# Kernel optimization log

Measured on AMD Instinct MI355X. Metric: run time of the kernel, lower is better.

## Reference

```python
import jax, jax.numpy as jnp
import numpy as np

NUM_MODULES = 4
EXPERTS_PER_MODULE = 4
TOTAL_EXPERTS = NUM_MODULES * EXPERTS_PER_MODULE
TOP_K = 4
NORM_TOPK_PROB = True
T = 32768
D = 1536


def setup_inputs() -> dict:
    key = jax.random.key(0)
    k1, k2, k3 = jax.random.split(key, 3)
    hidden_states = jax.random.normal(k1, (T, D), dtype=jnp.float32)
    # nn.Linear weights: (out_features, in_features)
    Wm = jax.random.normal(k2, (NUM_MODULES, D), dtype=jnp.float32) * 0.02
    We = jax.random.normal(k3, (TOTAL_EXPERTS, D), dtype=jnp.float32) * 0.02
    return {"hidden_states": hidden_states, "Wm": Wm, "We": We}


def reference(hidden_states, Wm, We):
    Tn = hidden_states.shape[0]
    # Stage 1: module routing
    module_logits = jnp.einsum('td,md->tm', hidden_states, Wm)  # (T, num_modules)
    module_probs = jax.nn.softmax(module_logits.astype(jnp.float32), axis=-1)
    # Stage 2: expert routing, grouped per module (intra-module softmax)
    expert_logits = jnp.einsum('td,ed->te', hidden_states, We)  # (T, total_experts)
    expert_logits = expert_logits.reshape(Tn, NUM_MODULES, EXPERTS_PER_MODULE)
    expert_probs = jax.nn.softmax(expert_logits.astype(jnp.float32), axis=-1)
    # Combined hierarchical distribution
    combined_probs = (module_probs[:, :, None] * expert_probs).reshape(Tn, TOTAL_EXPERTS)
    # Top-k over flat combined distribution
    top_k_weights, top_k_indices = jax.lax.top_k(combined_probs, TOP_K)
    if NORM_TOPK_PROB:
        top_k_weights = top_k_weights / (jnp.sum(top_k_weights, axis=-1, keepdims=True) + 1e-8)
    top_k_weights = top_k_weights.astype(hidden_states.dtype)
    return combined_probs, top_k_weights, top_k_indices
```

## Files before the change

### kernel.cpp

```cpp
#include <hip/hip_runtime.h>
#include <math.h>


#define DD 1536
#define NM 4
#define NE 16
#define NW 20
#define RPB 128
#define NWAVE 8
#define NTHR (NWAVE * 64)
#define CPW 192
#define CHUNK 16
#define HS_FLOATS (RPB * CHUNK)

typedef float v4f __attribute__((ext_vector_type(4)));

union SharedMem {
    float stage[NWAVE * HS_FLOATS];
    float xch[NW * NTHR * 2];
};

__global__ __launch_bounds__(NTHR)
void router_kernel(const float* __restrict__ hs,
                   const float* __restrict__ Wm,
                   const float* __restrict__ We,
                   float* __restrict__ out,
                   int T)
{
    __shared__ SharedMem sm;
    const int tid  = threadIdx.x;
    const int wv   = tid >> 6;
    const int lane = tid & 63;
    const int rowBlock = blockIdx.x * RPB;
    const int colStart = __builtin_amdgcn_readfirstlane(wv * CPW);

    float acc0[NW], acc1[NW];
#pragma unroll
    for (int e = 0; e < NW; e++) { acc0[e] = 0.f; acc1[e] = 0.f; }

    const int srow = lane >> 2;
    const int p    = lane & 3;
    const int sw   = (lane >> 3) & 3;
    const int gcol = ((p ^ sw) << 2);
    const float* dmaBase = hs + (size_t)(rowBlock + srow) * DD + colStart + gcol;

    const int myHsOff = __builtin_amdgcn_readfirstlane(wv * HS_FLOATS);
    const float* WeBase = We + colStart;
    const float* WmBase = Wm + colStart;
    const int rsw = ((lane >> 1) & 3);

    for (int c = 0; c < CPW; c += CHUNK) {
        asm volatile("s_waitcnt lgkmcnt(0)" ::: "memory");
#pragma unroll
        for (int i = 0; i < 8; i++) {
            const float* src = dmaBase + (size_t)(i * 16) * DD + c;
            __builtin_amdgcn_global_load_lds(
                (const __attribute__((address_space(1))) void*)src,
                (__attribute__((address_space(3))) void*)&sm.stage[myHsOff + i * 256],
                16, 0, 0);
        }
        asm volatile("s_waitcnt vmcnt(0)" ::: "memory");

#pragma unroll
        for (int g = 0; g < 4; g++) {
            const int sg = ((g ^ rsw) << 2);
            v4f h0 = *(const v4f*)&sm.stage[myHsOff + (lane << 4) + sg];
            v4f h1 = *(const v4f*)&sm.stage[myHsOff + 1024 + (lane << 4) + sg];
#pragma unroll
            for (int e = 0; e < NE; e++) {
                v4f w = *(const v4f*)(WeBase + e * DD + c + (g << 2));
                acc0[e] += h0.x * w.x + h0.y * w.y + h0.z * w.z + h0.w * w.w;
                acc1[e] += h1.x * w.x + h1.y * w.y + h1.z * w.z + h1.w * w.w;
            }
#pragma unroll
            for (int m = 0; m < NM; m++) {
                v4f w = *(const v4f*)(WmBase + m * DD + c + (g << 2));
                acc0[16 + m] += h0.x * w.x + h0.y * w.y + h0.z * w.z + h0.w * w.w;
                acc1[16 + m] += h1.x * w.x + h1.y * w.y + h1.z * w.z + h1.w * w.w;
            }
        }
    }

    __syncthreads();
#pragma unroll
    for (int e = 0; e < NW; e++) {
        sm.xch[e * (NTHR * 2) + tid]        = acc0[e];
        sm.xch[e * (NTHR * 2) + NTHR + tid] = acc1[e];
    }
    __syncthreads();

    if (wv < 2) {
        const int half = wv * NTHR;
        float logit[NW];
#pragma unroll
        for (int e = 0; e < NW; e++) {
            float s = 0.f;
#pragma unroll
            for (int w = 0; w < NWAVE; w++)
                s += sm.xch[e * (NTHR * 2) + half + w * 64 + lane];
            logit[e] = s;
        }

        float mmax = logit[16];
#pragma unroll
        for (int m = 1; m < NM; m++) mmax = fmaxf(mmax, logit[16 + m]);
        float mexp[NM], msum = 0.f;
#pragma unroll
        for (int m = 0; m < NM; m++) { mexp[m] = expf(logit[16 + m] - mmax); msum += mexp[m]; }

        float comb[NE];
#pragma unroll
        for (int m = 0; m < NM; m++) {
            float mprob = mexp[m] / msum;
            float emax = logit[m * 4];
#pragma unroll
            for (int j = 1; j < 4; j++) emax = fmaxf(emax, logit[m * 4 + j]);
            float ee[4], esum = 0.f;
#pragma unroll
            for (int j = 0; j < 4; j++) { ee[j] = expf(logit[m * 4 + j] - emax); esum += ee[j]; }
            float scale = mprob / esum;
#pragma unroll
            for (int j = 0; j < 4; j++) comb[m * 4 + j] = ee[j] * scale;
        }

        const int row = rowBlock + wv * 64 + lane;
        float4* cw = (float4*)(out + (size_t)row * 16);
        cw[0] = make_float4(comb[0],  comb[1],  comb[2],  comb[3]);
        cw[1] = make_float4(comb[4],  comb[5],  comb[6],  comb[7]);
        cw[2] = make_float4(comb[8],  comb[9],  comb[10], comb[11]);
        cw[3] = make_float4(comb[12], comb[13], comb[14], comb[15]);

        float tv[4]; int ti[4];
        unsigned mask = 0;
#pragma unroll
        for (int k = 0; k < 4; k++) {
            float best = -1.f; int bi = 0;
#pragma unroll
            for (int i = 0; i < NE; i++) {
                bool avail = !((mask >> i) & 1u);
                if (avail && comb[i] > best) { best = comb[i]; bi = i; }
            }
            tv[k] = best; ti[k] = bi; mask |= 1u << bi;
        }
        float s = tv[0] + tv[1] + tv[2] + tv[3] + 1e-8f;

        const size_t wOff = (size_t)T * 16;
        const size_t iOff = (size_t)T * 20;
        float4* ww = (float4*)(out + wOff + (size_t)row * 4);
        *ww = make_float4(tv[0] / s, tv[1] / s, tv[2] / s, tv[3] / s);
        float4* iw = (float4*)(out + iOff + (size_t)row * 4);
        *iw = make_float4((float)ti[0], (float)ti[1], (float)ti[2], (float)ti[3]);
    }
}

extern "C" void kernel_launch(void* const* d_in, const int* in_sizes, int n_in,
                              void* d_out, int out_size, void* d_ws, size_t ws_size,
                              hipStream_t stream)
{
    const float* hs = (const float*)d_in[0];
    const float* Wm = (const float*)d_in[1];
    const float* We = (const float*)d_in[2];
    float* out = (float*)d_out;
    const int T = in_sizes[0] / DD;
    router_kernel<<<T / RPB, NTHR, 0, stream>>>(hs, Wm, We, out, T);
}
```

Baseline: 362.3 us.

## Stage router weights in LDS and stream hidden states directly with shuffle reductions

Each block first copies all 20x1536 router weights (We and Wm) into LDS. Each wave then streams hidden-state rows straight from global memory with register prefetch, with 16 lanes splitting the columns of one row. Partial sums are combined with xor shuffles instead of a shared-memory cross-wave exchange. This removes the global_load_lds staging, the per-chunk waits and the large reduction buffer, but every block now reloads 120KB of weights and occupancy is limited by that LDS footprint.

```diff
diff --git a/kernel.cpp b/kernel.cpp
--- a/kernel.cpp
+++ b/kernel.cpp
@@ -7,18 +7,11 @@
 #define NE 16
 #define NW 20
 #define RPB 128
-#define NWAVE 8
-#define NTHR (NWAVE * 64)
-#define CPW 192
-#define CHUNK 16
-#define HS_FLOATS (RPB * CHUNK)
+#define NTHR 512
+#define NJ 24
+#define WLDS_F (NJ * NW * 64)
 
 typedef float v4f __attribute__((ext_vector_type(4)));
-
-union SharedMem {
-    float stage[NWAVE * HS_FLOATS];
-    float xch[NW * NTHR * 2];
-};
 
 __global__ __launch_bounds__(NTHR)
 void router_kernel(const float* __restrict__ hs,
@@ -27,129 +20,152 @@
                    float* __restrict__ out,
                    int T)
 {
-    __shared__ SharedMem sm;
+    __shared__ __align__(16) float wl[WLDS_F];
     const int tid  = threadIdx.x;
     const int wv   = tid >> 6;
     const int lane = tid & 63;
+    const int q    = lane & 15;
+    const int g    = lane >> 4;
     const int rowBlock = blockIdx.x * RPB;
-    const int colStart = __builtin_amdgcn_readfirstlane(wv * CPW);
-
-    float acc0[NW], acc1[NW];
-#pragma unroll
-    for (int e = 0; e < NW; e++) { acc0[e] = 0.f; acc1[e] = 0.f; }
-
-    const int srow = lane >> 2;
-    const int p    = lane & 3;
-    const int sw   = (lane >> 3) & 3;
-    const int gcol = ((p ^ sw) << 2);
-    const float* dmaBase = hs + (size_t)(rowBlock + srow) * DD + colStart + gcol;
-
-    const int myHsOff = __builtin_amdgcn_readfirstlane(wv * HS_FLOATS);
-    const float* WeBase = We + colStart;
-    const float* WmBase = Wm + colStart;
-    const int rsw = ((lane >> 1) & 3);
-
-    for (int c = 0; c < CPW; c += CHUNK) {
-        asm volatile("s_waitcnt lgkmcnt(0)" ::: "memory");
-#pragma unroll
-        for (int i = 0; i < 8; i++) {
-            const float* src = dmaBase + (size_t)(i * 16) * DD + c;
-            __builtin_amdgcn_global_load_lds(
-                (const __attribute__((address_space(1))) void*)src,
-                (__attribute__((address_space(3))) void*)&sm.stage[myHsOff + i * 256],
-                16, 0, 0);
-        }
-        asm volatile("s_waitcnt vmcnt(0)" ::: "memory");
 
 #pragma unroll
-        for (int g = 0; g < 4; g++) {
-            const int sg = ((g ^ rsw) << 2);
-            v4f h0 = *(const v4f*)&sm.stage[myHsOff + (lane << 4) + sg];
-            v4f h1 = *(const v4f*)&sm.stage[myHsOff + 1024 + (lane << 4) + sg];
-#pragma unroll
-            for (int e = 0; e < NE; e++) {
-                v4f w = *(const v4f*)(WeBase + e * DD + c + (g << 2));
-                acc0[e] += h0.x * w.x + h0.y * w.y + h0.z * w.z + h0.w * w.w;
-                acc1[e] += h1.x * w.x + h1.y * w.y + h1.z * w.z + h1.w * w.w;
-            }
-#pragma unroll
-            for (int m = 0; m < NM; m++) {
-                v4f w = *(const v4f*)(WmBase + m * DD + c + (g << 2));
-                acc0[16 + m] += h0.x * w.x + h0.y * w.y + h0.z * w.z + h0.w * w.w;
-                acc1[16 + m] += h1.x * w.x + h1.y * w.y + h1.z * w.z + h1.w * w.w;
-            }
-        }
-    }
-
-    __syncthreads();
-#pragma unroll
-    for (int e = 0; e < NW; e++) {
-        sm.xch[e * (NTHR * 2) + tid]        = acc0[e];
-        sm.xch[e * (NTHR * 2) + NTHR + tid] = acc1[e];
+    for (int i = 0; i < 15; i++) {
+        const int off  = tid * 4 + i * 2048;
+        const int j    = off / 1280;
+        const int rem  = off - j * 1280;
+        const int e    = rem >> 6;
+        const int qcol = rem & 63;
+        const int col  = j * 64 + qcol;
+        v4f w = (e < NE) ? *(const v4f*)(We + (size_t)e * DD + col)
+                         : *(const v4f*)(Wm + (size_t)(e - NE) * DD + col);
+        *(v4f*)&wl[off] = w;
     }
     __syncthreads();
 
-    if (wv < 2) {
-        const int half = wv * NTHR;
-        float logit[NW];
+#pragma unroll 1
+    for (int p = 0; p < 2; p++) {
+        const int rA = rowBlock + p * 64 + wv * 8 + g;
+        const float* hsA = hs + (size_t)rA * DD + q * 4;
+        const float* hsB = hsA + 4 * DD;
+
+        float accA[NW], accB[NW];
+#pragma unroll
+        for (int e = 0; e < NW; e++) { accA[e] = 0.f; accB[e] = 0.f; }
+
+        v4f a0 = *(const v4f*)(hsA);
+        v4f b0 = *(const v4f*)(hsB);
+        v4f a1 = *(const v4f*)(hsA + 64);
+        v4f b1 = *(const v4f*)(hsB + 64);
+
+#pragma unroll 1
+        for (int j = 0; j < NJ; j += 2) {
+            v4f a2, b2, a3, b3;
+            if (j + 2 < NJ) {
+                a2 = *(const v4f*)(hsA + (size_t)(j + 2) * 64);
+                b2 = *(const v4f*)(hsB + (size_t)(j + 2) * 64);
+                a3 = *(const v4f*)(hsA + (size_t)(j + 3) * 64);
+                b3 = *(const v4f*)(hsB + (size_t)(j + 3) * 64);
+            }
+            {
+                const float* wb = &wl[j * 1280 + q * 4];
+#pragma unroll
+                for (int e = 0; e < NW; e++) {
+                    v4f w = *(const v4f*)(wb + e * 64);
+                    accA[e] = fmaf(a0.x, w.x, accA[e]);
+                    accA[e] = fmaf(a0.y, w.y, accA[e]);
+                    accA[e] = fmaf(a0.z, w.z, accA[e]);
+                    accA[e] = fmaf(a0.w, w.w, accA[e]);
+                    accB[e] = fmaf(b0.x, w.x, accB[e]);
+                    accB[e] = fmaf(b0.y, w.y, accB[e]);
+                    accB[e] = fmaf(b0.z, w.z, accB[e]);
+                    accB[e] = fmaf(b0.w, w.w, accB[e]);
+                }
+            }
+            {
+                const float* wb = &wl[(j + 1) * 1280 + q * 4];
+#pragma unroll
+                for (int e = 0; e < NW; e++) {
+                    v4f w = *(const v4f*)(wb + e * 64);
+                    accA[e] = fmaf(a1.x, w.x, accA[e]);
+                    accA[e] = fmaf(a1.y, w.y, accA[e]);
+                    accA[e] = fmaf(a1.z, w.z, accA[e]);
+                    accA[e] = fmaf(a1.w, w.w, accA[e]);
+                    accB[e] = fmaf(b1.x, w.x, accB[e]);
+                    accB[e] = fmaf(b1.y, w.y, accB[e]);
+                    accB[e] = fmaf(b1.z, w.z, accB[e]);
+                    accB[e] = fmaf(b1.w, w.w, accB[e]);
+                }
+            }
+            a0 = a2; b0 = b2; a1 = a3; b1 = b3;
+        }
+
 #pragma unroll
         for (int e = 0; e < NW; e++) {
-            float s = 0.f;
-#pragma unroll
-            for (int w = 0; w < NWAVE; w++)
-                s += sm.xch[e * (NTHR * 2) + half + w * 64 + lane];
-            logit[e] = s;
+            accA[e] += __shfl_xor(accA[e], 1);
+            accA[e] += __shfl_xor(accA[e], 2);
+            accA[e] += __shfl_xor(accA[e], 4);
+            accA[e] += __shfl_xor(accA[e], 8);
+            accB[e] += __shfl_xor(accB[e], 1);
+            accB[e] += __shfl_xor(accB[e], 2);
+            accB[e] += __shfl_xor(accB[e], 4);
+            accB[e] += __shfl_xor(accB[e], 8);
         }
 
-        float mmax = logit[16];
+        if (q < 2) {
+            float logit[NW];
 #pragma unroll
-        for (int m = 1; m < NM; m++) mmax = fmaxf(mmax, logit[16 + m]);
-        float mexp[NM], msum = 0.f;
+            for (int e = 0; e < NW; e++) logit[e] = q ? accB[e] : accA[e];
+            const int row = rA + (q ? 4 : 0);
+
+            float mmax = logit[16];
 #pragma unroll
-        for (int m = 0; m < NM; m++) { mexp[m] = expf(logit[16 + m] - mmax); msum += mexp[m]; }
+            for (int m = 1; m < NM; m++) mmax = fmaxf(mmax, logit[16 + m]);
+            float mexp[NM], msum = 0.f;
+#pragma unroll
+            for (int m = 0; m < NM; m++) { mexp[m] = expf(logit[16 + m] - mmax); msum += mexp[m]; }
 
-        float comb[NE];
+            float comb[NE];
 #pragma unroll
-        for (int m = 0; m < NM; m++) {
-            float mprob = mexp[m] / msum;
-            float emax = logit[m * 4];
+            for (int m = 0; m < NM; m++) {
+                float mprob = mexp[m] / msum;
+                float emax = logit[m * 4];
 #pragma unroll
-            for (int j = 1; j < 4; j++) emax = fmaxf(emax, logit[m * 4 + j]);
-            float ee[4], esum = 0.f;
+                for (int jj = 1; jj < 4; jj++) emax = fmaxf(emax, logit[m * 4 + jj]);
+                float ee[4], esum = 0.f;
 #pragma unroll
-            for (int j = 0; j < 4; j++) { ee[j] = expf(logit[m * 4 + j] - emax); esum += ee[j]; }
-            float scale = mprob / esum;
+                for (int jj = 0; jj < 4; jj++) { ee[jj] = expf(logit[m * 4 + jj] - emax); esum += ee[jj]; }
+                float scale = mprob / esum;
 #pragma unroll
-            for (int j = 0; j < 4; j++) comb[m * 4 + j] = ee[j] * scale;
+                for (int jj = 0; jj < 4; jj++) comb[m * 4 + jj] = ee[jj] * scale;
+            }
+
+            float4* cw = (float4*)(out + (size_t)row * 16);
+            cw[0] = make_float4(comb[0],  comb[1],  comb[2],  comb[3]);
+            cw[1] = make_float4(comb[4],  comb[5],  comb[6],  comb[7]);
+            cw[2] = make_float4(comb[8],  comb[9],  comb[10], comb[11]);
+            cw[3] = make_float4(comb[12], comb[13], comb[14], comb[15]);
+
+            float tv[4]; int ti[4];
+            unsigned mask = 0;
+#pragma unroll
+            for (int k = 0; k < 4; k++) {
+                float best = -1.f; int bi = 0;
+#pragma unroll
+                for (int i = 0; i < NE; i++) {
+                    bool avail = !((mask >> i) & 1u);
+                    if (avail && comb[i] > best) { best = comb[i]; bi = i; }
+                }
+                tv[k] = best; ti[k] = bi; mask |= 1u << bi;
+            }
+            float s = tv[0] + tv[1] + tv[2] + tv[3] + 1e-8f;
+
+            const size_t wOff = (size_t)T * 16;
+            const size_t iOff = (size_t)T * 20;
+            float4* ww = (float4*)(out + wOff + (size_t)row * 4);
+            *ww = make_float4(tv[0] / s, tv[1] / s, tv[2] / s, tv[3] / s);
+            float4* iw = (float4*)(out + iOff + (size_t)row * 4);
+            *iw = make_float4((float)ti[0], (float)ti[1], (float)ti[2], (float)ti[3]);
         }
-
-        const int row = rowBlock + wv * 64 + lane;
-        float4* cw = (float4*)(out + (size_t)row * 16);
-        cw[0] = make_float4(comb[0],  comb[1],  comb[2],  comb[3]);
-        cw[1] = make_float4(comb[4],  comb[5],  comb[6],  comb[7]);
-        cw[2] = make_float4(comb[8],  comb[9],  comb[10], comb[11]);
-        cw[3] = make_float4(comb[12], comb[13], comb[14], comb[15]);
-
-        float tv[4]; int ti[4];
-        unsigned mask = 0;
-#pragma unroll
-        for (int k = 0; k < 4; k++) {
-            float best = -1.f; int bi = 0;
-#pragma unroll
-            for (int i = 0; i < NE; i++) {
-                bool avail = !((mask >> i) & 1u);
-                if (avail && comb[i] > best) { best = comb[i]; bi = i; }
-            }
-            tv[k] = best; ti[k] = bi; mask |= 1u << bi;
-        }
-        float s = tv[0] + tv[1] + tv[2] + tv[3] + 1e-8f;
-
-        const size_t wOff = (size_t)T * 16;
-        const size_t iOff = (size_t)T * 20;
-        float4* ww = (float4*)(out + wOff + (size_t)row * 4);
-        *ww = make_float4(tv[0] / s, tv[1] / s, tv[2] / s, tv[3] / s);
-        float4* iw = (float4*)(out + iOff + (size_t)row * 4);
-        *iw = make_float4((float)ti[0], (float)ti[1], (float)ti[2], (float)ti[3]);
     }
 }
 
```

Result: faster. 292.2 us (-19.3%).
